# Performance work log

Measured on AMD Instinct MI355X. Metric: run time of the kernel, lower is better.

## Reference

```python
import jax, jax.numpy as jnp
import numpy as np

GN_GROUPS = 32
GN_EPS = 1e-5


def conv3x3(x, w, b=None):
    # x: [B,C,H,W], w: [O,I,3,3]
    y = jax.lax.conv_general_dilated(x, w, (1, 1), 'SAME',
                                     dimension_numbers=('NCHW', 'OIHW', 'NCHW'))
    if b is not None:
        y = y + b[None, :, None, None]
    return y


def group_norm(x, gamma, beta):
    B, C, H, W = x.shape
    xg = x.reshape(B, GN_GROUPS, C // GN_GROUPS, H, W)
    mu = xg.mean(axis=(2, 3, 4), keepdims=True)
    var = ((xg - mu) ** 2).mean(axis=(2, 3, 4), keepdims=True)
    xn = ((xg - mu) * jax.lax.rsqrt(var + GN_EPS)).reshape(B, C, H, W)
    return xn * gamma[None, :, None, None] + beta[None, :, None, None]


def tower(x, ws, gammas, betas):
    # ws: [n_conv, C, C, 3, 3]; conv(bias=False) -> GroupNorm -> ReLU, n_conv times
    for i in range(ws.shape[0]):
        x = jax.nn.relu(group_norm(conv3x3(x, ws[i]), gammas[i], betas[i]))
    return x


def setup_inputs() -> dict:
    key = jax.random.key(0)
    ks = jax.random.split(key, 20)
    C, n_conv, n_fg = 256, 4, 20  # n_class - 1 = 20
    prior = 0.01
    B = 2
    sizes = [(100, 100), (50, 50), (25, 25), (13, 13), (7, 7)]
    inp = {}
    for i, (h, w) in enumerate(sizes):
        inp[f'feat{i}'] = jax.random.normal(ks[i], (B, C, h, w), dtype=jnp.float32)
    std = 0.01  # init_conv_std
    inp['cls_tw_w'] = std * jax.random.normal(ks[5], (n_conv, C, C, 3, 3), dtype=jnp.float32)
    inp['cls_tw_g'] = jnp.ones((n_conv, C), dtype=jnp.float32)
    inp['cls_tw_b'] = jnp.zeros((n_conv, C), dtype=jnp.float32)
    inp['box_tw_w'] = std * jax.random.normal(ks[6], (n_conv, C, C, 3, 3), dtype=jnp.float32)
    inp['box_tw_g'] = jnp.ones((n_conv, C), dtype=jnp.float32)
    inp['box_tw_b'] = jnp.zeros((n_conv, C), dtype=jnp.float32)
    inp['cls_pred_w'] = std * jax.random.normal(ks[7], (n_fg, C, 3, 3), dtype=jnp.float32)
    prior_bias = -np.log((1.0 - prior) / prior)
    inp['cls_pred_b'] = jnp.full((n_fg,), prior_bias, dtype=jnp.float32)
    inp['box_pred_w'] = std * jax.random.normal(ks[8], (4, C, 3, 3), dtype=jnp.float32)
    inp['box_pred_b'] = jnp.zeros((4,), dtype=jnp.float32)
    inp['ctr_pred_w'] = std * jax.random.normal(ks[9], (1, C, 3, 3), dtype=jnp.float32)
    inp['ctr_pred_b'] = jnp.zeros((1,), dtype=jnp.float32)
    inp['scales'] = jnp.ones((5,), dtype=jnp.float32)
    return inp


def reference(feat0, feat1, feat2, feat3, feat4,
              cls_tw_w, cls_tw_g, cls_tw_b,
              box_tw_w, box_tw_g, box_tw_b,
              cls_pred_w, cls_pred_b,
              box_pred_w, box_pred_b,
              ctr_pred_w, ctr_pred_b,
              scales):
    feats = [feat0, feat1, feat2, feat3, feat4]
    logits, bboxes, centers = [], [], []
    for i, feat in enumerate(feats):
        c = tower(feat, cls_tw_w, cls_tw_g, cls_tw_b)
        logits.append(conv3x3(c, cls_pred_w, cls_pred_b))
        centers.append(conv3x3(c, ctr_pred_w, ctr_pred_b))
        b = tower(feat, box_tw_w, box_tw_g, box_tw_b)
        bboxes.append(jnp.exp(conv3x3(b, box_pred_w, box_pred_b) * scales[i]))
    return tuple(logits + bboxes + centers)
```

## Files before the change

kernel.cpp:

```cpp
#include <hip/hip_runtime.h>
#include <hip/hip_bf16.h>
#include <cstdint>

typedef unsigned short u16;
typedef __attribute__((ext_vector_type(8))) short short8;
typedef __attribute__((ext_vector_type(4))) float floatx4;
typedef __attribute__((ext_vector_type(4))) int intx4;

#define PA_TOTAL 13696
#define CCH 256
#define KTOT 2304

struct Tables {
  int H[5], W[5], P[5], base[5], tile0[5];
  int lb[5], bb[5], cb[5];
};
struct FeatPtrs { const float* f[5]; };
struct ConvArgs {
  const u16* X[2];
  const u16* Wt[2];
  u16* outB[2];
  float* stats;
  float* dout;
  const float* biasCls; const float* biasCtr; const float* biasBox; const float* scales;
};
struct ReorderArgs {
  const float* cls_w; const float* box_w; const float* pcls_w; const float* ctr_w; const float* pbox_w;
  u16* wrCls; u16* wrBox; u16* wrPCls; u16* wrPBox;
};

__device__ __forceinline__ u16 f2bf(float f) {
  union { float f; unsigned u; } v; v.f = f;
  unsigned r = v.u + 0x7fffu + ((v.u >> 16) & 1u);
  return (u16)(r >> 16);
}
__device__ __forceinline__ float bf2f(u16 h) {
  union { unsigned u; float f; } v; v.u = ((unsigned)h) << 16;
  return v.f;
}

__device__ __forceinline__ void gload16(const void* g, void* l) {
  __builtin_amdgcn_global_load_lds(
      (const __attribute__((address_space(1))) void*)g,
      (__attribute__((address_space(3))) void*)l, 16, 0, 0);
}

__global__ void reorder_all(ReorderArgs ra) {
  __shared__ float row[KTOT];
  const int r = blockIdx.x;
  const float* s;
  u16* o;
  if (r < 1024)      { s = ra.cls_w  + (size_t)r * KTOT;          o = ra.wrCls  + (size_t)r * KTOT; }
  else if (r < 2048) { int q = r - 1024; s = ra.box_w  + (size_t)q * KTOT; o = ra.wrBox  + (size_t)q * KTOT; }
  else if (r < 2068) { int q = r - 2048; s = ra.pcls_w + (size_t)q * KTOT; o = ra.wrPCls + (size_t)q * KTOT; }
  else if (r == 2068){ s = ra.ctr_w;                               o = ra.wrPCls + (size_t)20 * KTOT; }
  else if (r < 2073) { int q = r - 2069; s = ra.pbox_w + (size_t)q * KTOT; o = ra.wrPBox + (size_t)q * KTOT; }
  else if (r < 2084) {
    u16* oz = ra.wrPCls + (size_t)(21 + (r - 2073)) * KTOT;
#pragma unroll
    for (int j = 0; j < 9; ++j) oz[threadIdx.x + j * 256] = 0;
    return;
  } else {
    u16* oz = ra.wrPBox + (size_t)(4 + (r - 2084)) * KTOT;
#pragma unroll
    for (int j = 0; j < 9; ++j) oz[threadIdx.x + j * 256] = 0;
    return;
  }
#pragma unroll
  for (int j = 0; j < 9; ++j) row[threadIdx.x + j * 256] = s[threadIdx.x + j * 256];
  __syncthreads();
#pragma unroll
  for (int j = 0; j < 9; ++j) {
    int k = threadIdx.x + j * 256;
    o[k] = f2bf(row[(k & 255) * 9 + (k >> 8)]);
  }
}

__global__ void convert_inputs(FeatPtrs fp, u16* __restrict__ out, Tables tb) {
  __shared__ float tile[32][33];
  const int pt = blockIdx.x, c32 = blockIdx.y, b = blockIdx.z;
  const int p0 = pt * 32;
  int lvl = 0;
#pragma unroll
  for (int i = 1; i < 5; ++i) if (p0 >= tb.base[i]) lvl = i;
  const int P = tb.P[lvl];
  const int pl0 = p0 - tb.base[lvl];
  const int r = threadIdx.x >> 5, col = threadIdx.x & 31;
  const float* src = fp.f[lvl] + ((size_t)b * CCH + c32 * 32) * P;
#pragma unroll
  for (int i = 0; i < 4; ++i) {
    int crow = r + i * 8;
    int pl = pl0 + col;
    tile[crow][col] = (pl < P) ? src[(size_t)crow * P + pl] : 0.f;
  }
  __syncthreads();
#pragma unroll
  for (int i = 0; i < 4; ++i) {
    int px = r + i * 8;
    out[((size_t)b * PA_TOTAL + p0 + px) * CCH + c32 * 32 + col] = f2bf(tile[col][px]);
  }
}

template <int MODE>
__global__ __launch_bounds__(256) void conv_mfma(ConvArgs a, Tables tb) {
  constexpr int NI = (MODE == 0) ? 4 : 1;
  constexpr int WROWS = (MODE == 0) ? 128 : 32;
  const int L = blockIdx.x + (MODE == 0 ? 107 : 108) * (blockIdx.y + 2 * blockIdx.z);
  const int xcd = L & 7, slot = L >> 3;
  int tower, mt, b, t;
  if (MODE == 0) {
    tower = xcd >> 2; mt = (xcd >> 1) & 1; b = xcd & 1; t = slot;
  } else {
    tower = xcd >> 2; mt = 0; b = (xcd >> 1) & 1; t = slot * 2 + (xcd & 1);
    if (t >= 107) return;
  }
  int lvl = 0;
#pragma unroll
  for (int i = 1; i < 5; ++i) if (t >= tb.tile0[i]) lvl = i;
  const int H = tb.H[lvl], W = tb.W[lvl], P = tb.P[lvl], base = tb.base[lvl];
  const int n0 = (t - tb.tile0[lvl]) * 128;

  const int tid = threadIdx.x;
  const int lane = tid & 63, wv = tid >> 6;
  const int wm = wv >> 1, wn = wv & 1;

  __shared__ u16 ldsAll[128 * 64 + WROWS * 64];
  u16* ldsX = ldsAll;
  u16* ldsW = ldsAll + 128 * 64;

  const u16* X = a.X[tower];
  const u16* Wt = a.Wt[tower];
  const char* Xb = (const char*)(X + ((size_t)b * PA_TOTAL + base) * CCH);
  const char* Wb = (const char*)(Wt + (size_t)(MODE == 0 ? mt * 128 : 0) * KTOT);

  const int qsw2 = ((lane & 7) ^ (lane >> 3)) * 16;
  int xoffG[4];
  unsigned mask9[4];
  int xlds[4];
#pragma unroll
  for (int t4 = 0; t4 < 4; ++t4) {
    int row = (t4 * 4 + wv) * 8 + (lane >> 3);
    int prow = n0 + row;
    int rr = prow / W, cc = prow - rr * W;
    unsigned m = 0;
#pragma unroll
    for (int tap = 0; tap < 9; ++tap) {
      const int dh = tap / 3 - 1, dw = tap % 3 - 1;
      bool v = ((unsigned)(rr + dh) < (unsigned)H) & ((unsigned)(cc + dw) < (unsigned)W);
      m |= ((unsigned)v) << tap;
    }
    mask9[t4] = m;
    xoffG[t4] = prow * (CCH * 2) + qsw2;
    xlds[t4] = (t4 * 4 + wv) * 1024;
  }
  const int padoff = P * (CCH * 2) + qsw2;
  int woffG[NI];
  int wlds[NI];
#pragma unroll
  for (int e = 0; e < NI; ++e) {
    int wrow = (MODE == 0) ? ((e * 4 + wv) * 8 + (lane >> 3)) : (wv * 8 + (lane >> 3));
    woffG[e] = wrow * (KTOT * 2) + qsw2;
    wlds[e] = 16384 + ((MODE == 0) ? ((e * 4 + wv) * 1024) : (wv * 1024));
  }

  const int arow = lane & 15, rsw = lane & 7, kq0 = lane >> 4;
  const int csw0 = (kq0 ^ rsw) * 8;
  int aoff[NI], boff[4];
#pragma unroll
  for (int i = 0; i < NI; ++i) {
    int rowb = (MODE == 0) ? (wm * 64 + i * 16) : (wm * 16);
    aoff[i] = (rowb + arow) * 64 + csw0;
  }
#pragma unroll
  for (int i = 0; i < 4; ++i) boff[i] = (wn * 64 + i * 16 + arow) * 64 + csw0;

  floatx4 acc[NI][4];
#pragma unroll
  for (int i = 0; i < NI; ++i)
#pragma unroll
    for (int j = 0; j < 4; ++j) acc[i][j] = (floatx4)0.f;

#pragma unroll 1
  for (int icb = 0; icb < 4; ++icb) {
#pragma unroll
    for (int tap = 0; tap < 9; ++tap) {
      __syncthreads();
      const int ko = (tap * 256 + icb * 64) * 2;
      const int dh = tap / 3 - 1, dw = tap % 3 - 1;
      const int doff = (dh * W + dw) * (CCH * 2) + icb * 128;
#pragma unroll
      for (int t4 = 0; t4 < 4; ++t4) {
        const int off = ((mask9[t4] >> tap) & 1u) ? (xoffG[t4] + doff) : padoff;
        gload16(Xb + off, (char*)ldsAll + xlds[t4]);
      }
#pragma unroll
      for (int e = 0; e < NI; ++e)
        gload16(Wb + woffG[e] + ko, (char*)ldsAll + wlds[e]);
      asm volatile("s_waitcnt vmcnt(0) lgkmcnt(0)\n\ts_barrier" ::: "memory");
      __builtin_amdgcn_s_setprio(1);
#pragma unroll
      for (int h = 0; h < 2; ++h) {
        const int hx = h * 32;
        short8 af[NI], bv[4];
#pragma unroll
        for (int i = 0; i < NI; ++i) af[i] = *(const short8*)(ldsW + (aoff[i] ^ hx));
#pragma unroll
        for (int j = 0; j < 4; ++j) bv[j] = *(const short8*)(ldsX + (boff[j] ^ hx));
#pragma unroll
        for (int i = 0; i < NI; ++i)
#pragma unroll
          for (int j = 0; j < 4; ++j)
            acc[i][j] = __builtin_amdgcn_mfma_f32_16x16x32_bf16(af[i], bv[j], acc[i][j], 0, 0, 0);
      }
      __builtin_amdgcn_s_setprio(0);
    }
  }

  const int quad = lane >> 4, col = lane & 15;
  if (MODE == 0) {
    u16* convB = a.outB[tower];
    float s[4] = {0.f, 0.f, 0.f, 0.f}, ss[4] = {0.f, 0.f, 0.f, 0.f};
#pragma unroll
    for (int j = 0; j < 4; ++j) {
      int pl = n0 + wn * 64 + j * 16 + col;
      bool valid = pl < P;
      u16* dst = convB + ((size_t)b * PA_TOTAL + base + pl) * CCH + mt * 128 + wm * 64 + quad * 4;
#pragma unroll
      for (int i = 0; i < 4; ++i) {
        ushort4 hv;
#pragma unroll
        for (int r = 0; r < 4; ++r) {
          u16 hh = f2bf(acc[i][j][r]);
          ((u16*)&hv)[r] = hh;
          float vr = bf2f(hh);
          if (valid) { s[i] += vr; ss[i] += vr * vr; }
        }
        if (valid) *(ushort4*)(dst + i * 16) = hv;
      }
    }
#pragma unroll
    for (int i = 0; i < 4; ++i) {
#pragma unroll
      for (int off = 16; off >= 1; off >>= 1) {
        s[i] += __shfl_down(s[i], off, 64);
        ss[i] += __shfl_down(ss[i], off, 64);
      }
    }
    if ((lane & 31) == 0) {
      int half = lane >> 5;
#pragma unroll
      for (int i = 0; i < 4; ++i) {
        float* st = a.stats + tower * 640 +
                    ((size_t)((b * 5 + lvl) * 32 + mt * 16 + wm * 8 + i * 2 + half)) * 2;
        atomicAdd(st, s[i]);
        atomicAdd(st + 1, ss[i]);
      }
    }
  } else {
    float* dout = a.dout;
    if (tower == 0) {
#pragma unroll
      for (int j = 0; j < 4; ++j) {
        int pl = n0 + wn * 64 + j * 16 + col;
        if (pl >= P) continue;
        int ocb = wm * 16 + quad * 4;
#pragma unroll
        for (int r = 0; r < 4; ++r) {
          int oc = ocb + r;
          float v = acc[0][j][r];
          if (oc < 20)       dout[tb.lb[lvl] + ((size_t)b * 20 + oc) * P + pl] = v + a.biasCls[oc];
          else if (oc == 20) dout[tb.cb[lvl] + (size_t)b * P + pl] = v + a.biasCtr[0];
        }
      }
    } else {
      float sc = a.scales[lvl];
#pragma unroll
      for (int j = 0; j < 4; ++j) {
        int pl = n0 + wn * 64 + j * 16 + col;
        if (pl >= P) continue;
        int ocb = wm * 16 + quad * 4;
#pragma unroll
        for (int r = 0; r < 4; ++r) {
          int oc = ocb + r;
          if (oc < 4)
            dout[tb.bb[lvl] + ((size_t)b * 4 + oc) * P + pl] = expf((acc[0][j][r] + a.biasBox[oc]) * sc);
        }
      }
    }
  }
}

__global__ void gn_norm(const u16* __restrict__ c0, const u16* __restrict__ c1,
                        const float* __restrict__ stats,
                        const float* __restrict__ g0, const float* __restrict__ b0,
                        const float* __restrict__ g1, const float* __restrict__ b1,
                        u16* __restrict__ a0, u16* __restrict__ a1, Tables tb) {
  const int tower = blockIdx.y;
  const u16* convB = tower ? c1 : c0;
  const float* gamma = tower ? g1 : g0;
  const float* beta = tower ? b1 : b0;
  u16* act = tower ? a1 : a0;
  int idx = blockIdx.x * 256 + threadIdx.x;
  int c8 = idx & 31;
  int rest = idx >> 5;
  int p = rest % PA_TOTAL;
  int b = rest / PA_TOTAL;
  int lvl = 0;
#pragma unroll
  for (int i = 1; i < 5; ++i) if (p >= tb.base[i]) lvl = i;
  if (p - tb.base[lvl] >= tb.P[lvl]) {
    short8 z = (short8)(short)0;
    *(short8*)(act + ((size_t)b * PA_TOTAL + p) * CCH + c8 * 8) = z;
    return;
  }
  const float* st = stats + tower * 640 + ((size_t)((b * 5 + lvl) * 32 + c8)) * 2;
  float cnt = 8.f * (float)tb.P[lvl];
  float mean = st[0] / cnt;
  float var = st[1] / cnt - mean * mean;
  float inv = rsqrtf(var + 1e-5f);
  const short8 x = *(const short8*)(convB + ((size_t)b * PA_TOTAL + p) * CCH + c8 * 8);
  short8 o;
#pragma unroll
  for (int j = 0; j < 8; ++j) {
    float v = bf2f((u16)x[j]);
    float y = (v - mean) * inv * gamma[c8 * 8 + j] + beta[c8 * 8 + j];
    y = fmaxf(y, 0.f);
    o[j] = (short)f2bf(y);
  }
  *(short8*)(act + ((size_t)b * PA_TOTAL + p) * CCH + c8 * 8) = o;
}

extern "C" void kernel_launch(void* const* d_in, const int* in_sizes, int n_in,
                              void* d_out, int out_size, void* d_ws, size_t ws_size,
                              hipStream_t stream) {
  const float* feat[5];
  for (int i = 0; i < 5; ++i) feat[i] = (const float*)d_in[i];
  const float* cls_tw_w  = (const float*)d_in[5];
  const float* cls_tw_g  = (const float*)d_in[6];
  const float* cls_tw_b  = (const float*)d_in[7];
  const float* box_tw_w  = (const float*)d_in[8];
  const float* box_tw_g  = (const float*)d_in[9];
  const float* box_tw_b  = (const float*)d_in[10];
  const float* cls_pred_w = (const float*)d_in[11];
  const float* cls_pred_b = (const float*)d_in[12];
  const float* box_pred_w = (const float*)d_in[13];
  const float* box_pred_b = (const float*)d_in[14];
  const float* ctr_pred_w = (const float*)d_in[15];
  const float* ctr_pred_b = (const float*)d_in[16];
  const float* scales     = (const float*)d_in[17];
  float* out = (float*)d_out;

  char* ws = (char*)d_ws;
  float* statsAll = (float*)(ws);
  u16*   WrCls  = (u16*)(ws + 24576);
  u16*   WrBox  = (u16*)(ws + 24576 + 4718592);
  u16*   WrPCls = (u16*)(ws + 24576 + 2 * 4718592);
  u16*   WrPBox = (u16*)(ws + 24576 + 2 * 4718592 + 147456);
  u16*   bufIn   = (u16*)(ws + 10625024);
  u16*   bufAct0 = (u16*)(ws + 10625024 + 1 * (size_t)14024704);
  u16*   bufAct1 = (u16*)(ws + 10625024 + 2 * (size_t)14024704);
  u16*   bufCv0  = (u16*)(ws + 10625024 + 3 * (size_t)14024704);
  u16*   bufCv1  = (u16*)(ws + 10625024 + 4 * (size_t)14024704);

  Tables tb = { {100,50,25,13,7}, {100,50,25,13,7}, {10000,2500,625,169,49},
                {0,10112,12672,13312,13568}, {0,79,99,104,106},
                {0,400000,500000,525000,531760},
                {533720,613720,633720,638720,640072},
                {640464,660464,665464,666714,667052} };

  hipMemsetAsync(statsAll, 0, 20480, stream);

  ReorderArgs ra = { cls_tw_w, box_tw_w, cls_pred_w, ctr_pred_w, box_pred_w,
                     WrCls, WrBox, WrPCls, WrPBox };
  reorder_all<<<2112, 256, 0, stream>>>(ra);

  FeatPtrs fp = {{feat[0], feat[1], feat[2], feat[3], feat[4]}};
  convert_inputs<<<dim3(PA_TOTAL / 32, 8, 2), 256, 0, stream>>>(fp, bufIn, tb);

  ConvArgs a;
  a.dout = out;
  a.biasCls = cls_pred_b; a.biasCtr = ctr_pred_b; a.biasBox = box_pred_b; a.scales = scales;
  a.outB[0] = bufCv0; a.outB[1] = bufCv1;

  for (int s = 0; s < 4; ++s) {
    a.X[0] = (s == 0) ? bufIn : bufAct0;
    a.X[1] = (s == 0) ? bufIn : bufAct1;
    a.Wt[0] = WrCls + (size_t)s * 256 * KTOT;
    a.Wt[1] = WrBox + (size_t)s * 256 * KTOT;
    a.stats = statsAll + (size_t)s * 1280;
    conv_mfma<0><<<dim3(107, 2, 4), 256, 0, stream>>>(a, tb);
    gn_norm<<<dim3(3424, 2), 256, 0, stream>>>(bufCv0, bufCv1, a.stats,
                                               cls_tw_g + s * 256, cls_tw_b + s * 256,
                                               box_tw_g + s * 256, box_tw_b + s * 256,
                                               bufAct0, bufAct1, tb);
  }
  a.X[0] = bufAct0; a.X[1] = bufAct1;
  a.Wt[0] = WrPCls; a.Wt[1] = WrPBox;
  conv_mfma<1><<<dim3(108, 2, 2), 256, 0, stream>>>(a, tb);
}
```

Measured before the change: 642.9 us.

## Double-buffer tower conv LDS tiles with 32-wide K slices and prefetch

Splits the templated conv kernel into a dedicated tower kernel and a prediction kernel. The tower kernel now uses two LDS buffers holding 32-channel K slices. While the MFMAs consume the current buffer, it issues the global-to-LDS loads for the next tap, waiting with a partial vmcnt and a raw s_barrier, so load latency overlaps compute. It also changes the XOR swizzle to fit the narrower slices. The cost is twice as many barrier and load rounds per block, with fewer MFMAs between each.

```diff
diff --git a/kernel.cpp b/kernel.cpp
--- a/kernel.cpp
+++ b/kernel.cpp
@@ -101,19 +101,10 @@
   }
 }
 
-template <int MODE>
-__global__ __launch_bounds__(256) void conv_mfma(ConvArgs a, Tables tb) {
-  constexpr int NI = (MODE == 0) ? 4 : 1;
-  constexpr int WROWS = (MODE == 0) ? 128 : 32;
-  const int L = blockIdx.x + (MODE == 0 ? 107 : 108) * (blockIdx.y + 2 * blockIdx.z);
+__global__ __launch_bounds__(256) void conv_tower(ConvArgs a, Tables tb) {
+  const int L = blockIdx.x + 107 * (blockIdx.y + 2 * blockIdx.z);
   const int xcd = L & 7, slot = L >> 3;
-  int tower, mt, b, t;
-  if (MODE == 0) {
-    tower = xcd >> 2; mt = (xcd >> 1) & 1; b = xcd & 1; t = slot;
-  } else {
-    tower = xcd >> 2; mt = 0; b = (xcd >> 1) & 1; t = slot * 2 + (xcd & 1);
-    if (t >= 107) return;
-  }
+  const int tower = xcd >> 2, mt = (xcd >> 1) & 1, b = xcd & 1, t = slot;
   int lvl = 0;
 #pragma unroll
   for (int i = 1; i < 5; ++i) if (t >= tb.tile0[i]) lvl = i;
@@ -124,14 +115,174 @@
   const int lane = tid & 63, wv = tid >> 6;
   const int wm = wv >> 1, wn = wv & 1;
 
+  __shared__ u16 ldsAll[2 * 8192];
+
+  const char* Xb = (const char*)(a.X[tower] + ((size_t)b * PA_TOTAL + base) * CCH);
+  const char* Wb = (const char*)(a.Wt[tower] + (size_t)(mt * 128) * KTOT);
+
+  const int qsw2 = (((lane & 3) ^ ((lane >> 2) & 3) ^ ((lane >> 4) & 3))) * 16;
+  int xoffG[2];
+  unsigned mask9[2];
+  int xl[2];
+#pragma unroll
+  for (int k = 0; k < 2; ++k) {
+    const int g = wv + 4 * k;
+    const int prow = n0 + 16 * g + (lane >> 2);
+    int rr = prow / W, cc = prow - rr * W;
+    unsigned m = 0;
+#pragma unroll
+    for (int tap = 0; tap < 9; ++tap) {
+      const int dh = tap / 3 - 1, dw = tap % 3 - 1;
+      bool v = ((unsigned)(rr + dh) < (unsigned)H) & ((unsigned)(cc + dw) < (unsigned)W);
+      m |= ((unsigned)v) << tap;
+    }
+    mask9[k] = m;
+    xoffG[k] = prow * 512 + qsw2;
+    xl[k] = g * 1024;
+  }
+  const int padbase = P * 512 + qsw2;
+  int woffG[2];
+#pragma unroll
+  for (int k = 0; k < 2; ++k) {
+    const int wrow = 16 * (wv + 4 * k) + (lane >> 2);
+    woffG[k] = wrow * (KTOT * 2) + qsw2;
+  }
+
+  const int arow = lane & 15, kq = lane >> 4;
+  const int csw0 = ((kq ^ (arow & 3) ^ ((arow >> 2) & 3))) * 16;
+  int rbA[4], rbX[4];
+#pragma unroll
+  for (int i = 0; i < 4; ++i) {
+    rbA[i] = (wm * 64 + i * 16 + arow) * 64 + csw0;
+    rbX[i] = (wn * 64 + i * 16 + arow) * 64 + csw0;
+  }
+
+  floatx4 acc[4][4];
+#pragma unroll
+  for (int i = 0; i < 4; ++i)
+#pragma unroll
+    for (int j = 0; j < 4; ++j) acc[i][j] = (floatx4)0.f;
+
+  {
+    const int doff0 = (-W - 1) * 512;
+#pragma unroll
+    for (int k = 0; k < 2; ++k) {
+      const int off = (mask9[k] & 1u) ? (xoffG[k] + doff0) : padbase;
+      gload16(Xb + off, (char*)ldsAll + xl[k]);
+    }
+#pragma unroll
+    for (int k = 0; k < 2; ++k)
+      gload16(Wb + woffG[k], (char*)ldsAll + 8192 + xl[k]);
+  }
+
+  int pb = 0;
+#pragma unroll 1
+  for (int icb2 = 0; icb2 < 8; ++icb2) {
+#pragma unroll
+    for (int tap = 0; tap < 9; ++tap) {
+      asm volatile("s_barrier" ::: "memory");
+      if (!(icb2 == 7 && tap == 8)) {
+        const int ntap = (tap == 8) ? 0 : tap + 1;
+        const int nic  = (tap == 8) ? icb2 + 1 : icb2;
+        const int ndh = ntap / 3;
+        const int ndoff = ((ndh - 1) * W + (ntap - 3 * ndh - 1)) * 512;
+        const int nslice = nic * 64;
+        char* bufN = (char*)ldsAll + (pb ^ 1) * 16384;
+#pragma unroll
+        for (int k = 0; k < 2; ++k) {
+          const int off = ((((mask9[k] >> ntap) & 1u) ? (xoffG[k] + ndoff) : padbase)) + nslice;
+          gload16(Xb + off, bufN + xl[k]);
+        }
+        const int nko = ntap * 512 + nslice;
+#pragma unroll
+        for (int k = 0; k < 2; ++k)
+          gload16(Wb + woffG[k] + nko, bufN + 8192 + xl[k]);
+        asm volatile("s_waitcnt vmcnt(4)\n\ts_barrier" ::: "memory");
+      } else {
+        asm volatile("s_waitcnt vmcnt(0)\n\ts_barrier" ::: "memory");
+      }
+      const char* bufc = (const char*)ldsAll + pb * 16384;
+      __builtin_amdgcn_s_setprio(1);
+      short8 af[4], bv[4];
+#pragma unroll
+      for (int i = 0; i < 4; ++i) af[i] = *(const short8*)(bufc + 8192 + rbA[i]);
+#pragma unroll
+      for (int j = 0; j < 4; ++j) bv[j] = *(const short8*)(bufc + rbX[j]);
+#pragma unroll
+      for (int i = 0; i < 4; ++i)
+#pragma unroll
+        for (int j = 0; j < 4; ++j)
+          acc[i][j] = __builtin_amdgcn_mfma_f32_16x16x32_bf16(af[i], bv[j], acc[i][j], 0, 0, 0);
+      __builtin_amdgcn_s_setprio(0);
+      pb ^= 1;
+    }
+  }
+
+  const int quad = lane >> 4, col = lane & 15;
+  u16* convB = a.outB[tower];
+  float s[4] = {0.f, 0.f, 0.f, 0.f}, ss[4] = {0.f, 0.f, 0.f, 0.f};
+#pragma unroll
+  for (int j = 0; j < 4; ++j) {
+    int pl = n0 + wn * 64 + j * 16 + col;
+    bool valid = pl < P;
+    u16* dst = convB + ((size_t)b * PA_TOTAL + base + pl) * CCH + mt * 128 + wm * 64 + quad * 4;
+#pragma unroll
+    for (int i = 0; i < 4; ++i) {
+      ushort4 hv;
+#pragma unroll
+      for (int r = 0; r < 4; ++r) {
+        u16 hh = f2bf(acc[i][j][r]);
+        ((u16*)&hv)[r] = hh;
+        float vr = bf2f(hh);
+        if (valid) { s[i] += vr; ss[i] += vr * vr; }
+      }
+      if (valid) *(ushort4*)(dst + i * 16) = hv;
+    }
+  }
+#pragma unroll
+  for (int i = 0; i < 4; ++i) {
+#pragma unroll
+    for (int off = 16; off >= 1; off >>= 1) {
+      s[i] += __shfl_down(s[i], off, 64);
+      ss[i] += __shfl_down(ss[i], off, 64);
+    }
+  }
+  if ((lane & 31) == 0) {
+    int half = lane >> 5;
+#pragma unroll
+    for (int i = 0; i < 4; ++i) {
+      float* st = a.stats + tower * 640 +
+                  ((size_t)((b * 5 + lvl) * 32 + mt * 16 + wm * 8 + i * 2 + half)) * 2;
+      atomicAdd(st, s[i]);
+      atomicAdd(st + 1, ss[i]);
+    }
+  }
+}
+
+__global__ __launch_bounds__(256) void conv_pred(ConvArgs a, Tables tb) {
+  constexpr int NI = 1;
+  constexpr int WROWS = 32;
+  const int L = blockIdx.x + 108 * (blockIdx.y + 2 * blockIdx.z);
+  const int xcd = L & 7, slot = L >> 3;
+  const int tower = xcd >> 2, b = (xcd >> 1) & 1;
+  const int t = slot * 2 + (xcd & 1);
+  if (t >= 107) return;
+  int lvl = 0;
+#pragma unroll
+  for (int i = 1; i < 5; ++i) if (t >= tb.tile0[i]) lvl = i;
+  const int H = tb.H[lvl], W = tb.W[lvl], P = tb.P[lvl], base = tb.base[lvl];
+  const int n0 = (t - tb.tile0[lvl]) * 128;
+
+  const int tid = threadIdx.x;
+  const int lane = tid & 63, wv = tid >> 6;
+  const int wm = wv >> 1, wn = wv & 1;
+
   __shared__ u16 ldsAll[128 * 64 + WROWS * 64];
   u16* ldsX = ldsAll;
   u16* ldsW = ldsAll + 128 * 64;
 
-  const u16* X = a.X[tower];
-  const u16* Wt = a.Wt[tower];
-  const char* Xb = (const char*)(X + ((size_t)b * PA_TOTAL + base) * CCH);
-  const char* Wb = (const char*)(Wt + (size_t)(MODE == 0 ? mt * 128 : 0) * KTOT);
+  const char* Xb = (const char*)(a.X[tower] + ((size_t)b * PA_TOTAL + base) * CCH);
+  const char* Wb = (const char*)(a.Wt[tower]);
 
   const int qsw2 = ((lane & 7) ^ (lane >> 3)) * 16;
   int xoffG[4];
@@ -158,19 +309,16 @@
   int wlds[NI];
 #pragma unroll
   for (int e = 0; e < NI; ++e) {
-    int wrow = (MODE == 0) ? ((e * 4 + wv) * 8 + (lane >> 3)) : (wv * 8 + (lane >> 3));
+    int wrow = wv * 8 + (lane >> 3);
     woffG[e] = wrow * (KTOT * 2) + qsw2;
-    wlds[e] = 16384 + ((MODE == 0) ? ((e * 4 + wv) * 1024) : (wv * 1024));
+    wlds[e] = 16384 + wv * 1024;
   }
 
   const int arow = lane & 15, rsw = lane & 7, kq0 = lane >> 4;
   const int csw0 = (kq0 ^ rsw) * 8;
   int aoff[NI], boff[4];
 #pragma unroll
-  for (int i = 0; i < NI; ++i) {
-    int rowb = (MODE == 0) ? (wm * 64 + i * 16) : (wm * 16);
-    aoff[i] = (rowb + arow) * 64 + csw0;
-  }
+  for (int i = 0; i < NI; ++i) aoff[i] = (wm * 16 + arow) * 64 + csw0;
 #pragma unroll
   for (int i = 0; i < 4; ++i) boff[i] = (wn * 64 + i * 16 + arow) * 64 + csw0;
 
@@ -217,74 +365,33 @@
   }
 
   const int quad = lane >> 4, col = lane & 15;
-  if (MODE == 0) {
-    u16* convB = a.outB[tower];
-    float s[4] = {0.f, 0.f, 0.f, 0.f}, ss[4] = {0.f, 0.f, 0.f, 0.f};
+  float* dout = a.dout;
+  if (tower == 0) {
 #pragma unroll
     for (int j = 0; j < 4; ++j) {
       int pl = n0 + wn * 64 + j * 16 + col;
-      bool valid = pl < P;
-      u16* dst = convB + ((size_t)b * PA_TOTAL + base + pl) * CCH + mt * 128 + wm * 64 + quad * 4;
-#pragma unroll
-      for (int i = 0; i < 4; ++i) {
-        ushort4 hv;
-#pragma unroll
-        for (int r = 0; r < 4; ++r) {
-          u16 hh = f2bf(acc[i][j][r]);
-          ((u16*)&hv)[r] = hh;
-          float vr = bf2f(hh);
-          if (valid) { s[i] += vr; ss[i] += vr * vr; }
-        }
-        if (valid) *(ushort4*)(dst + i * 16) = hv;
+      if (pl >= P) continue;
+      int ocb = wm * 16 + quad * 4;
+#pragma unroll
+      for (int r = 0; r < 4; ++r) {
+        int oc = ocb + r;
+        float v = acc[0][j][r];
+        if (oc < 20)       dout[tb.lb[lvl] + ((size_t)b * 20 + oc) * P + pl] = v + a.biasCls[oc];
+        else if (oc == 20) dout[tb.cb[lvl] + (size_t)b * P + pl] = v + a.biasCtr[0];
       }
     }
-#pragma unroll
-    for (int i = 0; i < 4; ++i) {
-#pragma unroll
-      for (int off = 16; off >= 1; off >>= 1) {
-        s[i] += __shfl_down(s[i], off, 64);
-        ss[i] += __shfl_down(ss[i], off, 64);
-      }
-    }
-    if ((lane & 31) == 0) {
-      int half = lane >> 5;
-#pragma unroll
-      for (int i = 0; i < 4; ++i) {
-        float* st = a.stats + tower * 640 +
-                    ((size_t)((b * 5 + lvl) * 32 + mt * 16 + wm * 8 + i * 2 + half)) * 2;
-        atomicAdd(st, s[i]);
-        atomicAdd(st + 1, ss[i]);
-      }
-    }
   } else {
-    float* dout = a.dout;
-    if (tower == 0) {
-#pragma unroll
-      for (int j = 0; j < 4; ++j) {
-        int pl = n0 + wn * 64 + j * 16 + col;
-        if (pl >= P) continue;
-        int ocb = wm * 16 + quad * 4;
-#pragma unroll
-        for (int r = 0; r < 4; ++r) {
-          int oc = ocb + r;
-          float v = acc[0][j][r];
-          if (oc < 20)       dout[tb.lb[lvl] + ((size_t)b * 20 + oc) * P + pl] = v + a.biasCls[oc];
-          else if (oc == 20) dout[tb.cb[lvl] + (size_t)b * P + pl] = v + a.biasCtr[0];
-        }
-      }
-    } else {
-      float sc = a.scales[lvl];
-#pragma unroll
-      for (int j = 0; j < 4; ++j) {
-        int pl = n0 + wn * 64 + j * 16 + col;
-        if (pl >= P) continue;
-        int ocb = wm * 16 + quad * 4;
-#pragma unroll
-        for (int r = 0; r < 4; ++r) {
-          int oc = ocb + r;
-          if (oc < 4)
-            dout[tb.bb[lvl] + ((size_t)b * 4 + oc) * P + pl] = expf((acc[0][j][r] + a.biasBox[oc]) * sc);
-        }
+    float sc = a.scales[lvl];
+#pragma unroll
+    for (int j = 0; j < 4; ++j) {
+      int pl = n0 + wn * 64 + j * 16 + col;
+      if (pl >= P) continue;
+      int ocb = wm * 16 + quad * 4;
+#pragma unroll
+      for (int r = 0; r < 4; ++r) {
+        int oc = ocb + r;
+        if (oc < 4)
+          dout[tb.bb[lvl] + ((size_t)b * 4 + oc) * P + pl] = expf((acc[0][j][r] + a.biasBox[oc]) * sc);
       }
     }
   }
@@ -388,7 +495,7 @@
     a.Wt[0] = WrCls + (size_t)s * 256 * KTOT;
     a.Wt[1] = WrBox + (size_t)s * 256 * KTOT;
     a.stats = statsAll + (size_t)s * 1280;
-    conv_mfma<0><<<dim3(107, 2, 4), 256, 0, stream>>>(a, tb);
+    conv_tower<<<dim3(107, 2, 4), 256, 0, stream>>>(a, tb);
     gn_norm<<<dim3(3424, 2), 256, 0, stream>>>(bufCv0, bufCv1, a.stats,
                                                cls_tw_g + s * 256, cls_tw_b + s * 256,
                                                box_tw_g + s * 256, box_tw_b + s * 256,
@@ -396,5 +503,5 @@
   }
   a.X[0] = bufAct0; a.X[1] = bufAct1;
   a.Wt[0] = WrPCls; a.Wt[1] = WrPBox;
-  conv_mfma<1><<<dim3(108, 2, 2), 256, 0, stream>>>(a, tb);
-}
+  conv_pred<<<dim3(108, 2, 2), 256, 0, stream>>>(a, tb);
+}
```

Result: faster. 609.4 us, median of 2 (-5.2%).
